# Performance work log

Hardware: AMD Instinct MI355X
Metric: run time of the kernel (lower is better)

## Reference

```python
import jax, jax.numpy as jnp
import numpy as np

NUM_HEADS = 12


def setup_inputs() -> dict:
    key = jax.random.key(0)
    k0, k1, k2 = jax.random.split(key, 3)
    B, N, C = 32, 864, 768  # N = 2*t_h*t_w + s_h*s_w = 288 + 576
    x = jax.random.normal(k0, (B, N, C), dtype=jnp.float32)
    W_qkv = jax.random.normal(k1, (C, 3 * C), dtype=jnp.float32) * 0.02
    W_proj = jax.random.normal(k2, (C, C), dtype=jnp.float32) * 0.02
    b_proj = jnp.zeros((C,), dtype=jnp.float32)
    return {"x": x, "W_qkv": W_qkv, "W_proj": W_proj, "b_proj": b_proj,
            "t_h": 12, "t_w": 12, "s_h": 24, "s_w": 24}


def reference(x, W_qkv, W_proj, b_proj, t_h, t_w, s_h, s_w):
    B, N, C = x.shape
    H = NUM_HEADS
    d = C // H
    scale = d ** -0.5
    # qkv projection (no bias), shape [3, B, H, N, d]
    qkv = (x @ W_qkv).reshape(B, N, 3, H, d).transpose(2, 0, 3, 1, 4)
    q, k, v = qkv[0], qkv[1], qkv[2]
    Tt = 2 * t_h * t_w            # temporal (template) query tokens = 288
    Ts = s_h * s_w                # spatial (search) query tokens = 576
    Mt = 2 * ((t_h + 1) // 2) ** 2  # sub-sampled temporal kv tokens = 72
    Ms = (s_h * s_w) // 4           # sub-sampled spatial kv tokens = 144
    q_t, q_s = q[:, :, :Tt], q[:, :, Tt:Tt + Ts]
    k_t, k_s = k[:, :, :Mt], k[:, :, Mt:Mt + Ms]
    v_t, v_s = v[:, :, :Mt], v[:, :, Mt:Mt + Ms]
    # temporal queries attend spatial keys/values
    a_t = jax.nn.softmax(jnp.einsum('bhqd,bhkd->bhqk', q_t, k_s) * scale, axis=-1)
    x_t = jnp.einsum('bhqk,bhkd->bhqd', a_t, v_s).transpose(0, 2, 1, 3).reshape(B, Tt, C)
    # spatial queries attend temporal keys/values
    a_s = jax.nn.softmax(jnp.einsum('bhqd,bhkd->bhqk', q_s, k_t) * scale, axis=-1)
    x_s = jnp.einsum('bhqk,bhkd->bhqd', a_s, v_t).transpose(0, 2, 1, 3).reshape(B, Ts, C)
    out = jnp.concatenate([x_t, x_s], axis=1)  # [B, N, C]
    return out @ W_proj + b_proj
```

## Files before the change

### kernel.cpp

```cpp
#include <hip/hip_runtime.h>
#include <hip/hip_bf16.h>

typedef __attribute__((ext_vector_type(8))) short short8;
typedef __attribute__((ext_vector_type(4))) float floatx4;

#define MFMA16(a, b, c) __builtin_amdgcn_mfma_f32_16x16x32_bf16((a), (b), (c), 0, 0, 0)

static constexpr int Bb = 32, Nn = 864, Cc = 768, Hh = 12;
static constexpr int Mm = Bb * Nn;
static constexpr int NQKV = 3 * Cc;
static constexpr int NKV = 2 * Cc;
static constexpr int KVROWS = 256;

__device__ __forceinline__ void gload_lds16(const __hip_bfloat16* g, __hip_bfloat16* l) {
    __builtin_amdgcn_global_load_lds((const __attribute__((address_space(1))) void*)g,
                                     (__attribute__((address_space(3))) void*)l, 16, 0, 0);
}

static constexpr int CVT_BLKS = (Mm * Cc / 4) / 256;
static constexpr int TQKV_BLKS = (NQKV / 32) * (Cc / 32);
static constexpr int TPROJ_BLKS = (Cc / 32) * (Cc / 32);

__global__ __launch_bounds__(256) void prep_kernel(const float* __restrict__ x,
                                                   const float* __restrict__ Wqkv,
                                                   const float* __restrict__ Wproj,
                                                   __hip_bfloat16* __restrict__ xb,
                                                   __hip_bfloat16* __restrict__ WqkvT,
                                                   __hip_bfloat16* __restrict__ WprojT) {
    __shared__ float tile[32][33];
    const int bx = blockIdx.x;
    if (bx < CVT_BLKS) {
        const int i = bx * 256 + threadIdx.x;
        const float4 v = ((const float4*)x)[i];
        __hip_bfloat16 o[4] = {__float2bfloat16(v.x), __float2bfloat16(v.y),
                               __float2bfloat16(v.z), __float2bfloat16(v.w)};
        ((uint2*)xb)[i] = *(const uint2*)o;
        return;
    }
    const float* in;
    __hip_bfloat16* out;
    int R, C, bid;
    if (bx < CVT_BLKS + TQKV_BLKS) {
        bid = bx - CVT_BLKS; in = Wqkv; out = WqkvT; R = Cc; C = NQKV;
    } else {
        bid = bx - CVT_BLKS - TQKV_BLKS; in = Wproj; out = WprojT; R = Cc; C = Cc;
    }
    const int c0 = (bid % (C / 32)) * 32, r0 = (bid / (C / 32)) * 32;
    const int tx = threadIdx.x & 31, ty = threadIdx.x >> 5;
#pragma unroll
    for (int i = 0; i < 32; i += 8)
        tile[ty + i][tx] = in[(size_t)(r0 + ty + i) * C + c0 + tx];
    __syncthreads();
#pragma unroll
    for (int i = 0; i < 32; i += 8)
        out[(size_t)(c0 + ty + i) * R + r0 + tx] = __float2bfloat16(tile[tx][ty + i]);
}

template <typename OutT, bool KVMODE>
__global__ __launch_bounds__(256) void gemm_bt(const __hip_bfloat16* __restrict__ A,
                                               const __hip_bfloat16* __restrict__ BT,
                                               OutT* __restrict__ Cout,
                                               const float* __restrict__ bias,
                                               int K, int Nout) {
    __shared__ __align__(16) __hip_bfloat16 As[8192];
    __shared__ __align__(16) __hip_bfloat16 Bs[8192];
    const int gx = (int)gridDim.x;
    const int nwg = gx * (int)gridDim.y;
    const int braw = (int)blockIdx.y * gx + (int)blockIdx.x;
    const int cpx = nwg >> 3;
    const int sid = (braw & 7) * cpx + (braw >> 3);
    const int mt = sid / gx, nt = sid - mt * gx;
    int arow0, orow0;
    if constexpr (KVMODE) {
        const int b = mt >> 1, r = (mt & 1) << 7;
        arow0 = b * Nn + r;
        orow0 = b * KVROWS + r;
    } else {
        arow0 = mt << 7;
        orow0 = arow0;
    }
    const int n0 = nt * 128;
    const int t = threadIdx.x;
    const int lane = t & 63, wave = t >> 6;
    const int wm = (wave >> 1) * 64, wn = (wave & 1) * 64;
    const int ln = lane & 15, quad = lane >> 4;

    floatx4 acc[4][4] = {};

    const int r0 = t >> 2;
    const int cst = (t & 3) * 8;
    const __hip_bfloat16* Ag = A + (size_t)(arow0 + r0) * K + cst;
    const __hip_bfloat16* Bg = BT + (size_t)(n0 + r0) * K + cst;
    const size_t rowskip = (size_t)64 * K;

    for (int k0 = 0; k0 < K; k0 += 64) {
        gload_lds16(Ag + k0,                &As[t * 8]);
        gload_lds16(Ag + k0 + rowskip,      &As[2048 + t * 8]);
        gload_lds16(Ag + k0 + 32,           &As[4096 + t * 8]);
        gload_lds16(Ag + k0 + 32 + rowskip, &As[6144 + t * 8]);
        gload_lds16(Bg + k0,                &Bs[t * 8]);
        gload_lds16(Bg + k0 + rowskip,      &Bs[2048 + t * 8]);
        gload_lds16(Bg + k0 + 32,           &Bs[4096 + t * 8]);
        gload_lds16(Bg + k0 + 32 + rowskip, &Bs[6144 + t * 8]);
        __syncthreads();

#pragma unroll
        for (int s = 0; s < 2; s++) {
            short8 af[4], bfr[4];
#pragma unroll
            for (int i = 0; i < 4; i++)
                af[i] = *(const short8*)&As[s * 4096 + (wm + i * 16 + ln) * 32 + quad * 8];
#pragma unroll
            for (int j = 0; j < 4; j++)
                bfr[j] = *(const short8*)&Bs[s * 4096 + (wn + j * 16 + ln) * 32 + quad * 8];
#pragma unroll
            for (int i = 0; i < 4; i++)
#pragma unroll
                for (int j = 0; j < 4; j++)
                    acc[i][j] = MFMA16(af[i], bfr[j], acc[i][j]);
        }
        __syncthreads();
    }

#pragma unroll
    for (int j = 0; j < 4; j++) {
        const int n = n0 + wn + j * 16 + ln;
        const float bv = bias ? bias[n] : 0.0f;
#pragma unroll
        for (int i = 0; i < 4; i++) {
            const int mrow = orow0 + wm + i * 16 + quad * 4;
#pragma unroll
            for (int r = 0; r < 4; r++) {
                const float val = acc[i][j][r] + bv;
                if constexpr (__is_same(OutT, float))
                    Cout[(size_t)(mrow + r) * Nout + n] = val;
                else
                    Cout[(size_t)(mrow + r) * Nout + n] = __float2bfloat16(val);
            }
        }
    }
}

template <int L, int QOFF, int KVOFF, int NQT, int NCH>
__device__ __forceinline__ void attn_part(const __hip_bfloat16* __restrict__ qb,
                                          const __hip_bfloat16* __restrict__ kv,
                                          __hip_bfloat16* __restrict__ attn,
                                          int qc, int h, int b,
                                          __hip_bfloat16* Ks, __hip_bfloat16* VTs) {
    constexpr int RSTG = ((L + 15) / 16) * 16;
    constexpr int KPAD = NCH * 32;
    constexpr int VSTR = KPAD + 8;
    const int t = threadIdx.x, lane = t & 63, wave = t >> 6;
    const int ln = lane & 15, quad = lane >> 4;
    const __hip_bfloat16 z16 = __float2bfloat16(0.0f);

    const __hip_bfloat16* kbase = kv + (size_t)(b * KVROWS + KVOFF) * NKV + h * 64;
    const __hip_bfloat16* vbase = kbase + Cc;

    for (int c = t; c < RSTG * 8; c += 256) {
        const int key = c >> 3, d0 = (c & 7) * 8;
        uint4 val = make_uint4(0u, 0u, 0u, 0u);
        if (key < L) val = *(const uint4*)(kbase + (size_t)key * NKV + d0);
        *(uint4*)&Ks[key * 72 + d0] = val;
    }
    for (int c = t; c < KPAD * 8; c += 256) {
        const int key = c >> 3, d0 = (c & 7) * 8;
        if (key < L) {
            uint4 raw = *(const uint4*)(vbase + (size_t)key * NKV + d0);
            const __hip_bfloat16* pv = (const __hip_bfloat16*)&raw;
#pragma unroll
            for (int jj = 0; jj < 8; jj++) VTs[(d0 + jj) * VSTR + key] = pv[jj];
        } else {
#pragma unroll
            for (int jj = 0; jj < 8; jj++) VTs[(d0 + jj) * VSTR + key] = z16;
        }
    }
    __syncthreads();

    const int qt = qc * 4 + wave;
    if (qt >= NQT) return;

    const __hip_bfloat16* qrow = qb + (size_t)(b * Nn + QOFF + qt * 16 + ln) * Cc + h * 64;
    const short8 aq0 = *(const short8*)(qrow + quad * 8);
    const short8 aq1 = *(const short8*)(qrow + 32 + quad * 8);

    float dsum = 0.0f;
    floatx4 acco[4] = {};
    constexpr float CSC = 0.18033688011112042f;

#pragma unroll
    for (int ch = 0; ch < NCH; ch++) {
        unsigned int pk[2][2];
#pragma unroll
        for (int ti2 = 0; ti2 < 2; ti2++) {
            const int ti = ch * 2 + ti2;
            if (ti * 16 >= L) {
                pk[ti2][0] = 0u; pk[ti2][1] = 0u;
                continue;
            }
            const __hip_bfloat16* krow = &Ks[(ti * 16 + ln) * 72];
            const short8 k0 = *(const short8*)(krow + quad * 8);
            const short8 k1 = *(const short8*)(krow + 32 + quad * 8);
            floatx4 s = {0.f, 0.f, 0.f, 0.f};
            s = MFMA16(k0, aq0, s);
            s = MFMA16(k1, aq1, s);
            float p[4];
#pragma unroll
            for (int r = 0; r < 4; r++) {
                float e = exp2f(s[r] * CSC);
                if (ti * 16 + 16 > L)
                    if (ti * 16 + quad * 4 + r >= L) e = 0.0f;
                p[r] = e;
                dsum += e;
            }
            const __hip_bfloat162 lo = __float22bfloat162_rn(make_float2(p[0], p[1]));
            const __hip_bfloat162 hi = __float22bfloat162_rn(make_float2(p[2], p[3]));
            pk[ti2][0] = *(const unsigned int*)&lo;
            pk[ti2][1] = *(const unsigned int*)&hi;
        }
        const int srcA = ln + ((quad & 1) << 5);
        const int srcB = srcA + 16;
        const unsigned int c0 = (unsigned int)__shfl((int)pk[0][0], srcA);
        const unsigned int c1 = (unsigned int)__shfl((int)pk[0][1], srcA);
        const unsigned int c2 = (unsigned int)__shfl((int)pk[0][0], srcB);
        const unsigned int c3 = (unsigned int)__shfl((int)pk[0][1], srcB);
        const unsigned int d0 = (unsigned int)__shfl((int)pk[1][0], srcA);
        const unsigned int d1 = (unsigned int)__shfl((int)pk[1][1], srcA);
        const unsigned int d2 = (unsigned int)__shfl((int)pk[1][0], srcB);
        const unsigned int d3 = (unsigned int)__shfl((int)pk[1][1], srcB);
        const bool hi2 = quad >= 2;
        union { unsigned int u[4]; short8 v; } pf;
        pf.u[0] = hi2 ? d0 : c0;
        pf.u[1] = hi2 ? d1 : c1;
        pf.u[2] = hi2 ? d2 : c2;
        pf.u[3] = hi2 ? d3 : c3;
#pragma unroll
        for (int j = 0; j < 4; j++) {
            const short8 vt = *(const short8*)&VTs[(j * 16 + ln) * VSTR + ch * 32 + quad * 8];
            acco[j] = MFMA16(vt, pf.v, acco[j]);
        }
    }

    dsum += __shfl_xor(dsum, 16);
    dsum += __shfl_xor(dsum, 32);
    const float inv = 1.0f / dsum;

    const size_t orow = (size_t)(b * Nn + QOFF + qt * 16 + ln) * 768 + h * 64;
#pragma unroll
    for (int j = 0; j < 4; j++) {
        const __hip_bfloat162 lo =
            __float22bfloat162_rn(make_float2(acco[j][0] * inv, acco[j][1] * inv));
        const __hip_bfloat162 hi =
            __float22bfloat162_rn(make_float2(acco[j][2] * inv, acco[j][3] * inv));
        uint2 o = make_uint2(*(const unsigned int*)&lo, *(const unsigned int*)&hi);
        *(uint2*)&attn[orow + j * 16 + quad * 4] = o;
    }
}

__global__ __launch_bounds__(256) void attn_fused(const __hip_bfloat16* __restrict__ qb,
                                                  const __hip_bfloat16* __restrict__ kv,
                                                  __hip_bfloat16* __restrict__ attn) {
    __shared__ __align__(16) __hip_bfloat16 Ks[144 * 72];
    __shared__ __align__(16) __hip_bfloat16 VTs[64 * 168];
    const int h = blockIdx.y, b = blockIdx.z;
    if (blockIdx.x < 5)
        attn_part<144, 0, 72, 18, 5>(qb, kv, attn, blockIdx.x, h, b, Ks, VTs);
    else
        attn_part<72, 288, 0, 36, 3>(qb, kv, attn, blockIdx.x - 5, h, b, Ks, VTs);
}

extern "C" void kernel_launch(void* const* d_in, const int* in_sizes, int n_in,
                              void* d_out, int out_size, void* d_ws, size_t ws_size,
                              hipStream_t stream) {
    const float* x     = (const float*)d_in[0];
    const float* Wqkv  = (const float*)d_in[1];
    const float* Wproj = (const float*)d_in[2];
    const float* bproj = (const float*)d_in[3];
    float* out = (float*)d_out;

    char* ws = (char*)d_ws;
    __hip_bfloat16* xb     = (__hip_bfloat16*)ws;
    __hip_bfloat16* WqkvT  = (__hip_bfloat16*)(ws + 42467328);
    __hip_bfloat16* WprojT = (__hip_bfloat16*)(ws + 46006272);
    __hip_bfloat16* Qbuf   = (__hip_bfloat16*)(ws + 47185920);
    __hip_bfloat16* KVbuf  = (__hip_bfloat16*)(ws + 89653248);
    __hip_bfloat16* attn   = (__hip_bfloat16*)ws;

    prep_kernel<<<CVT_BLKS + TQKV_BLKS + TPROJ_BLKS, 256, 0, stream>>>(x, Wqkv, Wproj, xb,
                                                                       WqkvT, WprojT);
    gemm_bt<__hip_bfloat16, false><<<dim3(Cc / 128, Mm / 128), 256, 0, stream>>>(
        xb, WqkvT, Qbuf, nullptr, Cc, Cc);
    gemm_bt<__hip_bfloat16, true><<<dim3(NKV / 128, Bb * KVROWS / 128), 256, 0, stream>>>(
        xb, WqkvT + (size_t)Cc * Cc, KVbuf, nullptr, Cc, NKV);
    attn_fused<<<dim3(14, Hh, Bb), 256, 0, stream>>>(Qbuf, KVbuf, attn);
    gemm_bt<float, false><<<dim3(Cc / 128, Mm / 128), 256, 0, stream>>>(attn, WprojT, out,
                                                                        bproj, Cc, Cc);
}
```

Measured before the change: 330.4 us.

## Drop K LDS staging, swizzle V^T columns, remap blocks for XCD locality

The attention kernel no longer stages K in shared memory. Each wave reads its K fragments straight from global memory, which halves LDS use, and the kernel asks for 5 blocks per CU through launch bounds. V^T stores and loads use a rotated column index to reduce LDS bank conflicts. Block IDs are remapped so that consecutive blocks on the same XCD share (head, batch) K/V data. The cost is repeated global or L2 reads of K by every wave, and more index arithmetic.

```diff
diff --git a/kernel.cpp b/kernel.cpp
--- a/kernel.cpp
+++ b/kernel.cpp
@@ -146,8 +146,7 @@
                                           const __hip_bfloat16* __restrict__ kv,
                                           __hip_bfloat16* __restrict__ attn,
                                           int qc, int h, int b,
-                                          __hip_bfloat16* Ks, __hip_bfloat16* VTs) {
-    constexpr int RSTG = ((L + 15) / 16) * 16;
+                                          __hip_bfloat16* VTs) {
     constexpr int KPAD = NCH * 32;
     constexpr int VSTR = KPAD + 8;
     const int t = threadIdx.x, lane = t & 63, wave = t >> 6;
@@ -157,22 +156,17 @@
     const __hip_bfloat16* kbase = kv + (size_t)(b * KVROWS + KVOFF) * NKV + h * 64;
     const __hip_bfloat16* vbase = kbase + Cc;
 
-    for (int c = t; c < RSTG * 8; c += 256) {
-        const int key = c >> 3, d0 = (c & 7) * 8;
-        uint4 val = make_uint4(0u, 0u, 0u, 0u);
-        if (key < L) val = *(const uint4*)(kbase + (size_t)key * NKV + d0);
-        *(uint4*)&Ks[key * 72 + d0] = val;
-    }
     for (int c = t; c < KPAD * 8; c += 256) {
-        const int key = c >> 3, d0 = (c & 7) * 8;
+        const int key = c >> 3, s8 = c & 7, d0 = s8 * 8;
+        const int colp = (key + 8 * s8) % KPAD;
         if (key < L) {
             uint4 raw = *(const uint4*)(vbase + (size_t)key * NKV + d0);
             const __hip_bfloat16* pv = (const __hip_bfloat16*)&raw;
 #pragma unroll
-            for (int jj = 0; jj < 8; jj++) VTs[(d0 + jj) * VSTR + key] = pv[jj];
+            for (int jj = 0; jj < 8; jj++) VTs[(d0 + jj) * VSTR + colp] = pv[jj];
         } else {
 #pragma unroll
-            for (int jj = 0; jj < 8; jj++) VTs[(d0 + jj) * VSTR + key] = z16;
+            for (int jj = 0; jj < 8; jj++) VTs[(d0 + jj) * VSTR + colp] = z16;
         }
     }
     __syncthreads();
@@ -198,7 +192,7 @@
                 pk[ti2][0] = 0u; pk[ti2][1] = 0u;
                 continue;
             }
-            const __hip_bfloat16* krow = &Ks[(ti * 16 + ln) * 72];
+            const __hip_bfloat16* krow = kbase + (size_t)(ti * 16 + ln) * NKV;
             const short8 k0 = *(const short8*)(krow + quad * 8);
             const short8 k1 = *(const short8*)(krow + 32 + quad * 8);
             floatx4 s = {0.f, 0.f, 0.f, 0.f};
@@ -236,7 +230,9 @@
         pf.u[3] = hi2 ? d3 : c3;
 #pragma unroll
         for (int j = 0; j < 4; j++) {
-            const short8 vt = *(const short8*)&VTs[(j * 16 + ln) * VSTR + ch * 32 + quad * 8];
+            const int dd = j * 16 + ln;
+            const int colp = (ch * 32 + quad * 8 + ((dd >> 3) << 3)) % KPAD;
+            const short8 vt = *(const short8*)&VTs[dd * VSTR + colp];
             acco[j] = MFMA16(vt, pf.v, acco[j]);
         }
     }
@@ -257,16 +253,19 @@
     }
 }
 
-__global__ __launch_bounds__(256) void attn_fused(const __hip_bfloat16* __restrict__ qb,
-                                                  const __hip_bfloat16* __restrict__ kv,
-                                                  __hip_bfloat16* __restrict__ attn) {
-    __shared__ __align__(16) __hip_bfloat16 Ks[144 * 72];
+__global__ __launch_bounds__(256, 5) void attn_fused(const __hip_bfloat16* __restrict__ qb,
+                                                     const __hip_bfloat16* __restrict__ kv,
+                                                     __hip_bfloat16* __restrict__ attn) {
     __shared__ __align__(16) __hip_bfloat16 VTs[64 * 168];
-    const int h = blockIdx.y, b = blockIdx.z;
-    if (blockIdx.x < 5)
-        attn_part<144, 0, 72, 18, 5>(qb, kv, attn, blockIdx.x, h, b, Ks, VTs);
+    constexpr int NB = 14 * 12 * 32;
+    const int rid = (int)blockIdx.x + 14 * ((int)blockIdx.y + 12 * (int)blockIdx.z);
+    const int vid = (rid & 7) * (NB / 8) + (rid >> 3);
+    const int qc = vid % 14, g = vid / 14;
+    const int h = g % 12, bq = g / 12;
+    if (qc < 5)
+        attn_part<144, 0, 72, 18, 5>(qb, kv, attn, qc, h, bq, VTs);
     else
-        attn_part<72, 288, 0, 36, 3>(qb, kv, attn, blockIdx.x - 5, h, b, Ks, VTs);
+        attn_part<72, 288, 0, 36, 3>(qb, kv, attn, qc - 5, h, bq, VTs);
 }
 
 extern "C" void kernel_launch(void* const* d_in, const int* in_sizes, int n_in,
```

New measurement: 334.4 us. About the same (+1.2%).
